# Kernel optimization log

Measured on AMD Instinct MI355X. Metric: run time of the kernel, lower is better.

Reference implementation:

```python
import jax, jax.numpy as jnp
import numpy as np

STRIDE = (16, 16)
PADDING = (0, 0)


def setup_inputs() -> dict:
    key = jax.random.key(0)
    k1, k2, k3 = jax.random.split(key, 3)
    x = jax.random.normal(k1, (16, 12, 512, 512), dtype=jnp.float32)
    weight = jax.random.normal(k2, (768, 1, 16, 16), dtype=jnp.float32) * 0.02
    bias = jax.random.normal(k3, (768,), dtype=jnp.float32) * 0.02
    return {"x": x, "weight": weight, "bias": bias}


def reference(x, weight, bias):
    # Faithful to the torch module: groups=c conv with the shared filter
    # repeated per input channel, then mean over the channel axis, then bias.
    b, c, h, w = x.shape
    o = weight.shape[0]
    # groups=c conv with repeated weight == independent conv of each channel
    # with the same (o,1,kh,kw) filter; fold channels into batch.
    xc = x.reshape(b * c, 1, h, w)
    y = jax.lax.conv_general_dilated(
        xc, weight,
        window_strides=STRIDE,
        padding=[(PADDING[0], PADDING[0]), (PADDING[1], PADDING[1])],
        dimension_numbers=("NCHW", "OIHW", "NCHW"),
    )  # (b*c, o, H', W')
    hp, wp = y.shape[-2], y.shape[-1]
    y = y.reshape(b, c, o, hp, wp).mean(axis=1)  # (b, o, H', W')
    y = y + bias[None, :, None, None]
    return y
```

## Files before the change

### kernel.cpp

```cpp
#include <hip/hip_runtime.h>
#include <hip/hip_bf16.h>

#define BATCH 16
#define CIN   12
#define HIMG  512
#define WIMG  512
#define OCH   768
#define KDIM  256
#define HW    (HIMG*WIMG)
#define NPATCH 1024
#define M_TOT (BATCH*NPATCH)

typedef __attribute__((ext_vector_type(8))) short short8;
typedef __attribute__((ext_vector_type(4))) float f32x4;

__global__ void wconv_kernel(const float* __restrict__ w, __hip_bfloat16* __restrict__ wb) {
    int idx = (blockIdx.x * blockDim.x + threadIdx.x) * 4;
    float4 v = *reinterpret_cast<const float4*>(w + idx);
    union { ushort4 u4; __hip_bfloat16 h[4]; } o;
    o.h[0] = __float2bfloat16(v.x);
    o.h[1] = __float2bfloat16(v.y);
    o.h[2] = __float2bfloat16(v.z);
    o.h[3] = __float2bfloat16(v.w);
    *reinterpret_cast<ushort4*>(wb + idx) = o.u4;
}

__global__ void mean_kernel(const float* __restrict__ x, __hip_bfloat16* __restrict__ xm) {
    int idx = blockIdx.x * blockDim.x + threadIdx.x;
    int b = idx >> 16;
    int pos = (idx & 65535) << 2;
    const float* px = x + (size_t)b * CIN * HW + pos;
    float sx = 0.f, sy = 0.f, sz = 0.f, sw = 0.f;
    #pragma unroll
    for (int c = 0; c < CIN; ++c) {
        float4 v = *reinterpret_cast<const float4*>(px + (size_t)c * HW);
        sx += v.x; sy += v.y; sz += v.z; sw += v.w;
    }
    const float inv = 1.0f / 12.0f;
    union { ushort4 u4; __hip_bfloat16 h[4]; } o;
    o.h[0] = __float2bfloat16(sx * inv);
    o.h[1] = __float2bfloat16(sy * inv);
    o.h[2] = __float2bfloat16(sz * inv);
    o.h[3] = __float2bfloat16(sw * inv);
    *reinterpret_cast<ushort4*>(xm + (size_t)idx * 4) = o.u4;
}

#define BO 64
#define BM 128
#define BK 64
#define LDK 72

__global__ __launch_bounds__(256) void gemm_kernel(
        const __hip_bfloat16* __restrict__ wb,
        const __hip_bfloat16* __restrict__ xm,
        const float* __restrict__ bias,
        float* __restrict__ out) {
    __shared__ short Al[BO][LDK];
    __shared__ short Bl[BM][LDK];

    const int mb = blockIdx.x;
    const int ob = blockIdx.y;
    const int m0 = mb * BM;
    const int o0 = ob * BO;
    const int tid  = threadIdx.x;
    const int lane = tid & 63;
    const int wv = tid >> 6;
    const int wo = wv >> 1;
    const int wm = wv & 1;
    const int lrow = lane & 15;
    const int lg   = lane >> 4;

    const int b  = m0 >> 10;
    const int p0 = m0 & 1023;

    const int srow  = tid >> 1;
    const int shalf = tid & 1;
    const int pm = p0 + srow;
    const int pi = pm >> 5;
    const int pj = pm & 31;
    const __hip_bfloat16* xbase =
        xm + (size_t)b * HW + (size_t)(pi * 16) * WIMG + pj * 16 + shalf * 8;

    const int arow = tid >> 2;
    const int aq   = tid & 3;
    const __hip_bfloat16* wbase = wb + (size_t)(o0 + arow) * KDIM + aq * 16;

    f32x4 acc[2][4] = {};

    for (int kc = 0; kc < 4; ++kc) {
        const int k0 = kc * BK;
        {
            const short* src = reinterpret_cast<const short*>(wbase + k0);
            *reinterpret_cast<short8*>(&Al[arow][aq * 16])     = *reinterpret_cast<const short8*>(src);
            *reinterpret_cast<short8*>(&Al[arow][aq * 16 + 8]) = *reinterpret_cast<const short8*>(src + 8);
        }
        {
            const int rc = kc * 4;
            #pragma unroll
            for (int dr = 0; dr < 4; ++dr) {
                const short* src = reinterpret_cast<const short*>(xbase + (size_t)(rc + dr) * WIMG);
                *reinterpret_cast<short8*>(&Bl[srow][dr * 16 + shalf * 8]) =
                    *reinterpret_cast<const short8*>(src);
            }
        }
        __syncthreads();
        #pragma unroll
        for (int kk = 0; kk < 2; ++kk) {
            short8 af[2], bf[4];
            #pragma unroll
            for (int fo = 0; fo < 2; ++fo)
                af[fo] = *reinterpret_cast<const short8*>(&Al[wo * 32 + fo * 16 + lrow][kk * 32 + lg * 8]);
            #pragma unroll
            for (int fm = 0; fm < 4; ++fm)
                bf[fm] = *reinterpret_cast<const short8*>(&Bl[wm * 64 + fm * 16 + lrow][kk * 32 + lg * 8]);
            #pragma unroll
            for (int fo = 0; fo < 2; ++fo)
                #pragma unroll
                for (int fm = 0; fm < 4; ++fm)
                    acc[fo][fm] = __builtin_amdgcn_mfma_f32_16x16x32_bf16(af[fo], bf[fm], acc[fo][fm], 0, 0, 0);
        }
        __syncthreads();
    }

    #pragma unroll
    for (int fo = 0; fo < 2; ++fo) {
        const int obase = o0 + wo * 32 + fo * 16 + lg * 4;
        #pragma unroll
        for (int r = 0; r < 4; ++r) {
            const int o = obase + r;
            const float bv = bias[o];
            float* orow = out + (size_t)b * (OCH * NPATCH) + (size_t)o * NPATCH + p0;
            #pragma unroll
            for (int fm = 0; fm < 4; ++fm)
                orow[wm * 64 + fm * 16 + lrow] = acc[fo][fm][r] + bv;
        }
    }
}

extern "C" void kernel_launch(void* const* d_in, const int* in_sizes, int n_in,
                              void* d_out, int out_size, void* d_ws, size_t ws_size,
                              hipStream_t stream) {
    const float* x    = (const float*)d_in[0];
    const float* w    = (const float*)d_in[1];
    const float* bias = (const float*)d_in[2];
    float* out = (float*)d_out;

    __hip_bfloat16* xm = (__hip_bfloat16*)d_ws;
    __hip_bfloat16* wbq = (__hip_bfloat16*)((char*)d_ws + (size_t)BATCH * HW * 2);

    wconv_kernel<<<OCH * KDIM / (256 * 4), 256, 0, stream>>>(w, wbq);
    mean_kernel<<<BATCH * HW / 4 / 256, 256, 0, stream>>>(x, xm);
    dim3 grid(M_TOT / BM, OCH / BO);
    gemm_kernel<<<grid, 256, 0, stream>>>(wbq, xm, bias, out);
}
```

Measured before the change: 56.52 us.

## Fuse channel-mean into GEMM and prepack weights in MFMA fragment order

The channel-mean kernel is folded into the GEMM. Each block reduces one 16-row strip of one image across the 12 channels directly into LDS, then multiplies it against all 768 output channels. Weights are prepacked into MFMA fragment order so each wave reads them straight from global or L2, with no LDS staging. This drops the bf16 mean intermediate's write and reread and removes one launch. The cost is that each block now streams the full weight matrix from cache and the grid is smaller (512 blocks of 512 threads).

```diff
diff --git a/kernel.cpp b/kernel.cpp
--- a/kernel.cpp
+++ b/kernel.cpp
@@ -9,130 +9,109 @@
 #define KDIM  256
 #define HW    (HIMG*WIMG)
 #define NPATCH 1024
-#define M_TOT (BATCH*NPATCH)
 
 typedef __attribute__((ext_vector_type(8))) short short8;
 typedef __attribute__((ext_vector_type(4))) float f32x4;
 
-__global__ void wconv_kernel(const float* __restrict__ w, __hip_bfloat16* __restrict__ wb) {
-    int idx = (blockIdx.x * blockDim.x + threadIdx.x) * 4;
-    float4 v = *reinterpret_cast<const float4*>(w + idx);
-    union { ushort4 u4; __hip_bfloat16 h[4]; } o;
-    o.h[0] = __float2bfloat16(v.x);
-    o.h[1] = __float2bfloat16(v.y);
-    o.h[2] = __float2bfloat16(v.z);
-    o.h[3] = __float2bfloat16(v.w);
-    *reinterpret_cast<ushort4*>(wb + idx) = o.u4;
+__global__ void wpack_kernel(const float* __restrict__ w, short8* __restrict__ wbp) {
+    int u = blockIdx.x * 256 + threadIdx.x;
+    int lane = u & 63;
+    int kk   = (u >> 6) & 7;
+    int ot   = u >> 9;
+    int o = ot * 16 + (lane & 15);
+    int k = kk * 32 + (lane >> 4) * 8;
+    const float* src = w + (size_t)o * KDIM + k;
+    float4 v0 = *reinterpret_cast<const float4*>(src);
+    float4 v1 = *reinterpret_cast<const float4*>(src + 4);
+    union { short8 s; __hip_bfloat16 h[8]; } t;
+    t.h[0] = __float2bfloat16(v0.x);
+    t.h[1] = __float2bfloat16(v0.y);
+    t.h[2] = __float2bfloat16(v0.z);
+    t.h[3] = __float2bfloat16(v0.w);
+    t.h[4] = __float2bfloat16(v1.x);
+    t.h[5] = __float2bfloat16(v1.y);
+    t.h[6] = __float2bfloat16(v1.z);
+    t.h[7] = __float2bfloat16(v1.w);
+    wbp[u] = t.s;
 }
 
-__global__ void mean_kernel(const float* __restrict__ x, __hip_bfloat16* __restrict__ xm) {
-    int idx = blockIdx.x * blockDim.x + threadIdx.x;
-    int b = idx >> 16;
-    int pos = (idx & 65535) << 2;
-    const float* px = x + (size_t)b * CIN * HW + pos;
-    float sx = 0.f, sy = 0.f, sz = 0.f, sw = 0.f;
-    #pragma unroll
-    for (int c = 0; c < CIN; ++c) {
-        float4 v = *reinterpret_cast<const float4*>(px + (size_t)c * HW);
-        sx += v.x; sy += v.y; sz += v.z; sw += v.w;
+#define LDB 264
+
+__global__ __launch_bounds__(512, 4) void fused_kernel(
+        const short8* __restrict__ wbp,
+        const float*  __restrict__ x,
+        const float*  __restrict__ bias,
+        float* __restrict__ out) {
+    __shared__ short Bl[32][LDB];
+
+    const int tid = threadIdx.x;
+    const int b  = blockIdx.x >> 5;
+    const int is = blockIdx.x & 31;
+
+    {
+        const int col = (tid & 127) * 4;
+        const int r0  = tid >> 7;
+        const int j   = col >> 4;
+        const int s0  = col & 15;
+        const float* xb = x + (size_t)b * CIN * HW + (size_t)(is * 16) * WIMG + col;
+        const float inv = 1.0f / 12.0f;
+        #pragma unroll
+        for (int p = 0; p < 4; ++p) {
+            const int r = p * 4 + r0;
+            const float* px = xb + (size_t)r * WIMG;
+            float sx = 0.f, sy = 0.f, sz = 0.f, sw = 0.f;
+            #pragma unroll
+            for (int c = 0; c < CIN; ++c) {
+                float4 v = *reinterpret_cast<const float4*>(px + (size_t)c * HW);
+                sx += v.x; sy += v.y; sz += v.z; sw += v.w;
+            }
+            union { ushort4 u4; __hip_bfloat16 h[4]; } o;
+            o.h[0] = __float2bfloat16(sx * inv);
+            o.h[1] = __float2bfloat16(sy * inv);
+            o.h[2] = __float2bfloat16(sz * inv);
+            o.h[3] = __float2bfloat16(sw * inv);
+            *reinterpret_cast<ushort4*>(&Bl[j][r * 16 + s0]) = o.u4;
+        }
     }
-    const float inv = 1.0f / 12.0f;
-    union { ushort4 u4; __hip_bfloat16 h[4]; } o;
-    o.h[0] = __float2bfloat16(sx * inv);
-    o.h[1] = __float2bfloat16(sy * inv);
-    o.h[2] = __float2bfloat16(sz * inv);
-    o.h[3] = __float2bfloat16(sw * inv);
-    *reinterpret_cast<ushort4*>(xm + (size_t)idx * 4) = o.u4;
-}
+    __syncthreads();
 
-#define BO 64
-#define BM 128
-#define BK 64
-#define LDK 72
-
-__global__ __launch_bounds__(256) void gemm_kernel(
-        const __hip_bfloat16* __restrict__ wb,
-        const __hip_bfloat16* __restrict__ xm,
-        const float* __restrict__ bias,
-        float* __restrict__ out) {
-    __shared__ short Al[BO][LDK];
-    __shared__ short Bl[BM][LDK];
-
-    const int mb = blockIdx.x;
-    const int ob = blockIdx.y;
-    const int m0 = mb * BM;
-    const int o0 = ob * BO;
-    const int tid  = threadIdx.x;
     const int lane = tid & 63;
-    const int wv = tid >> 6;
-    const int wo = wv >> 1;
-    const int wm = wv & 1;
+    const int wv   = tid >> 6;
     const int lrow = lane & 15;
     const int lg   = lane >> 4;
 
-    const int b  = m0 >> 10;
-    const int p0 = m0 & 1023;
+    f32x4 acc[6][2] = {};
+    const short8* wp = wbp + (size_t)(wv * 6) * 8 * 64 + lane;
 
-    const int srow  = tid >> 1;
-    const int shalf = tid & 1;
-    const int pm = p0 + srow;
-    const int pi = pm >> 5;
-    const int pj = pm & 31;
-    const __hip_bfloat16* xbase =
-        xm + (size_t)b * HW + (size_t)(pi * 16) * WIMG + pj * 16 + shalf * 8;
-
-    const int arow = tid >> 2;
-    const int aq   = tid & 3;
-    const __hip_bfloat16* wbase = wb + (size_t)(o0 + arow) * KDIM + aq * 16;
-
-    f32x4 acc[2][4] = {};
-
-    for (int kc = 0; kc < 4; ++kc) {
-        const int k0 = kc * BK;
-        {
-            const short* src = reinterpret_cast<const short*>(wbase + k0);
-            *reinterpret_cast<short8*>(&Al[arow][aq * 16])     = *reinterpret_cast<const short8*>(src);
-            *reinterpret_cast<short8*>(&Al[arow][aq * 16 + 8]) = *reinterpret_cast<const short8*>(src + 8);
-        }
-        {
-            const int rc = kc * 4;
+    #pragma unroll
+    for (int kk = 0; kk < 8; ++kk) {
+        short8 af[6], bf[2];
+        #pragma unroll
+        for (int fo = 0; fo < 6; ++fo)
+            af[fo] = wp[(size_t)(fo * 8 + kk) * 64];
+        #pragma unroll
+        for (int fm = 0; fm < 2; ++fm)
+            bf[fm] = *reinterpret_cast<const short8*>(&Bl[fm * 16 + lrow][kk * 32 + lg * 8]);
+        #pragma unroll
+        for (int fo = 0; fo < 6; ++fo)
             #pragma unroll
-            for (int dr = 0; dr < 4; ++dr) {
-                const short* src = reinterpret_cast<const short*>(xbase + (size_t)(rc + dr) * WIMG);
-                *reinterpret_cast<short8*>(&Bl[srow][dr * 16 + shalf * 8]) =
-                    *reinterpret_cast<const short8*>(src);
-            }
-        }
-        __syncthreads();
-        #pragma unroll
-        for (int kk = 0; kk < 2; ++kk) {
-            short8 af[2], bf[4];
-            #pragma unroll
-            for (int fo = 0; fo < 2; ++fo)
-                af[fo] = *reinterpret_cast<const short8*>(&Al[wo * 32 + fo * 16 + lrow][kk * 32 + lg * 8]);
-            #pragma unroll
-            for (int fm = 0; fm < 4; ++fm)
-                bf[fm] = *reinterpret_cast<const short8*>(&Bl[wm * 64 + fm * 16 + lrow][kk * 32 + lg * 8]);
-            #pragma unroll
-            for (int fo = 0; fo < 2; ++fo)
-                #pragma unroll
-                for (int fm = 0; fm < 4; ++fm)
-                    acc[fo][fm] = __builtin_amdgcn_mfma_f32_16x16x32_bf16(af[fo], bf[fm], acc[fo][fm], 0, 0, 0);
-        }
-        __syncthreads();
+            for (int fm = 0; fm < 2; ++fm)
+                acc[fo][fm] = __builtin_amdgcn_mfma_f32_16x16x32_bf16(af[fo], bf[fm], acc[fo][fm], 0, 0, 0);
     }
 
+    const int p0 = is * 32;
+    float* ob = out + (size_t)b * OCH * NPATCH + p0;
     #pragma unroll
-    for (int fo = 0; fo < 2; ++fo) {
-        const int obase = o0 + wo * 32 + fo * 16 + lg * 4;
+    for (int fo = 0; fo < 6; ++fo) {
+        const int obase = wv * 96 + fo * 16 + lg * 4;
         #pragma unroll
         for (int r = 0; r < 4; ++r) {
             const int o = obase + r;
             const float bv = bias[o];
-            float* orow = out + (size_t)b * (OCH * NPATCH) + (size_t)o * NPATCH + p0;
+            float* orow = ob + (size_t)o * NPATCH;
             #pragma unroll
-            for (int fm = 0; fm < 4; ++fm)
-                orow[wm * 64 + fm * 16 + lrow] = acc[fo][fm][r] + bv;
+            for (int fm = 0; fm < 2; ++fm)
+                orow[fm * 16 + lrow] = acc[fo][fm][r] + bv;
         }
     }
 }
@@ -145,11 +124,8 @@
     const float* bias = (const float*)d_in[2];
     float* out = (float*)d_out;
 
-    __hip_bfloat16* xm = (__hip_bfloat16*)d_ws;
-    __hip_bfloat16* wbq = (__hip_bfloat16*)((char*)d_ws + (size_t)BATCH * HW * 2);
+    short8* wbp = (short8*)d_ws;
 
-    wconv_kernel<<<OCH * KDIM / (256 * 4), 256, 0, stream>>>(w, wbq);
-    mean_kernel<<<BATCH * HW / 4 / 256, 256, 0, stream>>>(x, xm);
-    dim3 grid(M_TOT / BM, OCH / BO);
-    gemm_kernel<<<grid, 256, 0, stream>>>(wbq, xm, bias, out);
+    wpack_kernel<<<96, 256, 0, stream>>>(w, wbp);
+    fused_kernel<<<BATCH * 32, 512, 0, stream>>>(wbp, x, bias, out);
 }
```

Result: faster. 53.51 us (-5.3%).
